# Kernel optimization log

Hardware: AMD Instinct MI355X
Metric: run time of the kernel (lower is better)

## Reference

```python
import jax, jax.numpy as jnp
import numpy as np

N = 100000          # nodes
E = 800000          # edges per relation
R = 6               # relations
B = 1000            # graphs
IN_DIM = 14
POS_COL = 5
PE = 8              # pos_emb_dim
H = 128             # hidden_dim
OUT = 128           # out_dim
NPOS = 24
D1 = IN_DIM - 1 + PE  # 21, GAT layer-1 input dim


def setup_inputs() -> dict:
    key = jax.random.key(0)
    ks = jax.random.split(key, 20)
    x_all = jax.random.normal(ks[0], (N, IN_DIM), dtype=jnp.float32)
    pos = jax.random.randint(ks[1], (N,), 0, NPOS)
    x_all = x_all.at[:, POS_COL].set(pos.astype(jnp.float32))
    edges = jax.random.randint(ks[2], (R, 2, E), 0, N, dtype=jnp.int32)
    batch = jnp.sort(jax.random.randint(ks[3], (N,), 0, B, dtype=jnp.int32))
    pos_table = jax.random.normal(ks[4], (NPOS, PE), dtype=jnp.float32) * 0.02
    W1 = jax.random.normal(ks[5], (R, D1, H), dtype=jnp.float32) * 0.1
    as1 = jax.random.normal(ks[6], (R, H), dtype=jnp.float32) * 0.1
    ad1 = jax.random.normal(ks[7], (R, H), dtype=jnp.float32) * 0.1
    b1 = jnp.zeros((R, H), dtype=jnp.float32)
    W2 = jax.random.normal(ks[8], (R, H, H), dtype=jnp.float32) * 0.05
    as2 = jax.random.normal(ks[9], (R, H), dtype=jnp.float32) * 0.1
    ad2 = jax.random.normal(ks[10], (R, H), dtype=jnp.float32) * 0.1
    b2 = jnp.zeros((R, H), dtype=jnp.float32)
    n1w = jnp.ones((H,), dtype=jnp.float32)
    n1b = jnp.zeros((H,), dtype=jnp.float32)
    n2w = jnp.ones((H,), dtype=jnp.float32)
    n2b = jnp.zeros((H,), dtype=jnp.float32)
    query = jax.random.normal(ks[11], (H,), dtype=jnp.float32) * 0.02
    projW = jax.random.normal(ks[12], (H, OUT), dtype=jnp.float32) * 0.05
    projb = jnp.zeros((OUT,), dtype=jnp.float32)
    return dict(x_all=x_all, edges=edges, batch=batch, pos_table=pos_table,
                W1=W1, as1=as1, ad1=ad1, b1=b1, W2=W2, as2=as2, ad2=ad2, b2=b2,
                n1w=n1w, n1b=n1b, n2w=n2w, n2b=n2b, query=query, projW=projW, projb=projb)


def _seg_softmax(logits, seg, num):
    m = jax.lax.stop_gradient(jax.ops.segment_max(logits, seg, num_segments=num))
    e = jnp.exp(logits - m[seg])
    s = jax.ops.segment_sum(e, seg, num_segments=num)
    return e / s[seg]


def _gat_layer(x, W, a_s, a_d, b, edges):
    # sum over R relation-specific GATConv(heads=1, concat=False) outputs
    n = x.shape[0]
    out = jnp.zeros((n, W.shape[-1]), dtype=x.dtype)
    for r in range(R):
        xp = x @ W[r]                       # [N, H] projected features
        src, dst = edges[r, 0], edges[r, 1]
        z = (xp @ a_s[r])[src] + (xp @ a_d[r])[dst]
        z = jnp.where(z > 0, z, 0.2 * z)    # LeakyReLU(0.2)
        alpha = _seg_softmax(z, dst, n)     # per-destination softmax
        agg = jax.ops.segment_sum(alpha[:, None] * xp[src], dst, num_segments=n)
        out = out + agg + b[r]
    return out


def _ln(x, w, b):
    mu = x.mean(-1, keepdims=True)
    v = ((x - mu) ** 2).mean(-1, keepdims=True)
    return (x - mu) / jnp.sqrt(v + 1e-5) * w + b


def reference(x_all, edges, batch, pos_table, W1, as1, ad1, b1,
              W2, as2, ad2, b2, n1w, n1b, n2w, n2b, query, projW, projb):
    cont = jnp.concatenate([x_all[:, :POS_COL], x_all[:, POS_COL + 1:]], axis=1)
    pidx = jnp.clip(x_all[:, POS_COL].astype(jnp.int32), 0, NPOS - 1)
    x = jnp.concatenate([cont, pos_table[pidx]], axis=1)  # [N, D1]
    x = _gat_layer(x, W1, as1, ad1, b1, edges)
    x = _ln(jax.nn.gelu(x, approximate=False), n1w, n1b)
    x = _gat_layer(x, W2, as2, ad2, b2, edges)
    x = _ln(jax.nn.gelu(x, approximate=False), n2w, n2b)
    # AttentionPooling: gather-score-softmax-scatter over batch segments
    scores = x @ query
    w = _seg_softmax(scores, batch, B)
    pool = jax.ops.segment_sum(w[:, None] * x, batch, num_segments=B)  # [B, H]
    return pool @ projW + projb
```

## Files before the change

### kernel.cpp

```cpp
#include <hip/hip_runtime.h>
#include <math.h>

#define NN   100000
#define EE   800000
#define RR   6
#define BB   1000
#define HH   128
#define MM   (RR*NN)
#define NBPR ((NN + 255) >> 8)
#define NBK  (RR * NBPR)
#define CH   4096

static inline int ceil_div(int a, int b){ return (a+b-1)/b; }

typedef __attribute__((ext_vector_type(8))) short bf16x8;
typedef __attribute__((ext_vector_type(4))) short bf16x4;
typedef __attribute__((ext_vector_type(4))) float f32x4;

__device__ __forceinline__ unsigned fenc(float f){
  unsigned u = __float_as_uint(f);
  return (u & 0x80000000u) ? ~u : (u | 0x80000000u);
}
__device__ __forceinline__ float fdec(unsigned u){
  return __uint_as_float((u & 0x80000000u) ? (u & 0x7fffffffu) : ~u);
}
__device__ __forceinline__ unsigned short f2bf(float f){
  unsigned u = __float_as_uint(f);
  return (unsigned short)((u + 0x7fffu + ((u >> 16) & 1u)) >> 16);
}
__device__ __forceinline__ float bf2f(unsigned short h){
  return __uint_as_float(((unsigned)h) << 16);
}

__global__ void k_bcount(const int* __restrict__ edges, int* __restrict__ bcnt)
{
  __shared__ int hist[NBPR];
  int t = threadIdx.x;
  const int nch = (EE + CH - 1) / CH;
  int r = blockIdx.x / nch, c = blockIdx.x - r*nch;
  for (int i = t; i < NBPR; i += 256) hist[i] = 0;
  __syncthreads();
  const int* dptr = edges + (size_t)r*2*EE + EE;
  int e0 = c*CH, e1 = min(EE, e0 + CH);
  for (int i = e0 + t; i < e1; i += 256)
    atomicAdd(&hist[dptr[i] >> 8], 1);
  __syncthreads();
  for (int i = t; i < NBPR; i += 256) {
    int h = hist[i];
    if (h) atomicAdd(&bcnt[r*NBPR + i], h);
  }
}

__global__ void k_bscan(const int* __restrict__ bcnt, int* __restrict__ boff,
                        int* __restrict__ off)
{
  __shared__ int sh[256];
  int t = threadIdx.x;
  int carry = 0;
  for (int c = 0; c < NBK; c += 256) {
    int idx = c + t;
    int v = (idx < NBK) ? bcnt[idx] : 0;
    sh[t] = v;
    __syncthreads();
    for (int o = 1; o < 256; o <<= 1) {
      int add = (t >= o) ? sh[t-o] : 0;
      __syncthreads();
      sh[t] += add;
      __syncthreads();
    }
    int incl = sh[t];
    int tot  = sh[255];
    if (idx < NBK) boff[idx] = carry + incl - v;
    __syncthreads();
    carry += tot;
  }
  if (t == 0) { boff[NBK] = carry; off[MM] = carry; }
}

__global__ void k_binscatter(const int* __restrict__ edges, int* __restrict__ bcur,
                             unsigned* __restrict__ ebkt)
{
  __shared__ int hist[NBPR];
  __shared__ int base[NBPR];
  int t = threadIdx.x;
  const int nch = (EE + CH - 1) / CH;
  int r = blockIdx.x / nch, c = blockIdx.x - r*nch;
  for (int i = t; i < NBPR; i += 256) hist[i] = 0;
  __syncthreads();
  const int* sptr = edges + (size_t)r*2*EE;
  const int* dptr = sptr + EE;
  int e0 = c*CH, e1 = min(EE, e0 + CH);
  for (int i = e0 + t; i < e1; i += 256)
    atomicAdd(&hist[dptr[i] >> 8], 1);
  __syncthreads();
  for (int i = t; i < NBPR; i += 256) {
    int h = hist[i];
    base[i] = h ? atomicAdd(&bcur[r*NBPR + i], h) : 0;
    hist[i] = 0;
  }
  __syncthreads();
  for (int i = e0 + t; i < e1; i += 256) {
    int dst = dptr[i];
    int b = dst >> 8;
    int slot = base[b] + atomicAdd(&hist[b], 1);
    ebkt[slot] = ((unsigned)sptr[i] << 8) | (unsigned)(dst & 255);
  }
}

__global__ void k_bbuild(const unsigned* __restrict__ ebkt, const int* __restrict__ boff,
                         int* __restrict__ off, int* __restrict__ elist)
{
  __shared__ int cnt[256];
  __shared__ int sc[256];
  __shared__ int cur[256];
  int t = threadIdx.x;
  int bb = blockIdx.x;
  int e0 = boff[bb], e1 = boff[bb+1];
  cnt[t] = 0;
  __syncthreads();
  for (int i = e0 + t; i < e1; i += 256)
    atomicAdd(&cnt[ebkt[i] & 255u], 1);
  __syncthreads();
  sc[t] = cnt[t];
  __syncthreads();
  for (int o = 1; o < 256; o <<= 1) {
    int add = (t >= o) ? sc[t-o] : 0;
    __syncthreads();
    sc[t] += add;
    __syncthreads();
  }
  int excl = sc[t] - cnt[t];
  int r = bb / NBPR, b = bb - r*NBPR;
  int dst = b*256 + t;
  if (dst < NN) off[r*NN + dst] = e0 + excl;
  cur[t] = e0 + excl;
  __syncthreads();
  for (int i = e0 + t; i < e1; i += 256) {
    unsigned w = ebkt[i];
    int slot = atomicAdd(&cur[w & 255u], 1);
    elist[slot] = (int)(w >> 8);
  }
}

__global__ void k_featprep(const float* __restrict__ x_all, const float* __restrict__ pos_table,
                           short* __restrict__ x0h, short* __restrict__ x0l)
{
  int gid = blockIdx.x*256 + threadIdx.x;
  if (gid >= NN*32) return;
  int nidx = gid >> 5, c = gid & 31;
  float v = 0.f;
  if (c < 13) {
    int scl = (c < 5) ? c : c + 1;
    v = x_all[nidx*14 + scl];
  } else if (c < 21) {
    int pi = (int)x_all[nidx*14 + 5];
    pi = pi < 0 ? 0 : (pi > 23 ? 23 : pi);
    v = pos_table[pi*8 + (c - 13)];
  }
  unsigned short h = f2bf(v);
  unsigned short l = f2bf(v - bf2f(h));
  x0h[gid] = (short)h;
  x0l[gid] = (short)l;
}

template<int KP>
__global__ void k_wprep(const float* __restrict__ W, int K,
                        short* __restrict__ Wh, short* __restrict__ Wl)
{
  int gid = blockIdx.x*256 + threadIdx.x;
  if (gid >= RR*128*KP) return;
  int r = gid / (128*KP);
  int rem = gid - r*(128*KP);
  int nn = rem / KP, k = rem - nn*KP;
  float v = (k < K) ? W[((size_t)r*K + k)*128 + nn] : 0.f;
  unsigned short h = f2bf(v);
  unsigned short l = f2bf(v - bf2f(h));
  Wh[gid] = (short)h;
  Wl[gid] = (short)l;
}

template<int KP>
__global__ void k_wa(const float* __restrict__ W, const float* __restrict__ as,
                     const float* __restrict__ ad, int K, float* __restrict__ wa)
{
  int idx = blockIdx.x*256 + threadIdx.x;
  if (idx >= 12*KP) return;
  int rr = idx / KP, k = idx - rr*KP;
  int r = (rr < 6) ? rr : rr - 6;
  const float* a = ((rr < 6) ? as : ad) + (size_t)r*HH;
  float s = 0.f;
  if (k < K) {
    const float* wrow = W + ((size_t)r*K + k)*128;
    #pragma unroll 8
    for (int h = 0; h < 128; ++h) s = fmaf(wrow[h], a[h], s);
  }
  wa[idx] = s;
}

__global__ void k_zsd32(const short* __restrict__ xh, const short* __restrict__ xl,
                        const float* __restrict__ wa, float* __restrict__ zsd, int n)
{
  __shared__ float w[12*32];
  int tid = threadIdx.x;
  for (int i = tid; i < 12*32; i += 256) w[i] = wa[i];
  __syncthreads();
  int g = blockIdx.x*256 + tid;
  if (g >= n) return;
  float v[32];
  #pragma unroll
  for (int c = 0; c < 4; ++c) {
    uint4 vh = *(const uint4*)(xh + (size_t)g*32 + c*8);
    uint4 vl = *(const uint4*)(xl + (size_t)g*32 + c*8);
    const unsigned short* hp = (const unsigned short*)&vh;
    const unsigned short* lp = (const unsigned short*)&vl;
    #pragma unroll
    for (int j = 0; j < 8; ++j) v[c*8+j] = bf2f(hp[j]) + bf2f(lp[j]);
  }
  #pragma unroll
  for (int rr = 0; rr < 12; ++rr) {
    float d = 0.f;
    #pragma unroll
    for (int k = 0; k < 32; ++k) d = fmaf(v[k], w[rr*32+k], d);
    zsd[(size_t)rr*n + g] = d;
  }
}

__global__ void k_agg1(const unsigned short* __restrict__ x0h, const float* __restrict__ zsd,
                       const int* __restrict__ elist, const int* __restrict__ off,
                       unsigned short* __restrict__ aggH, unsigned short* __restrict__ aggL,
                       int n)
{
  int gid = blockIdx.x*256 + threadIdx.x;
  int g = gid >> 4;
  int l = threadIdx.x & 15;
  if (g >= n) return;
  int sub = l >> 2, ch = l & 3;

  for (int rel = 0; rel < RR; ++rel) {
    const float* zsr = zsd + (size_t)rel*n;
    const float* zdr = zsd + (size_t)(6+rel)*n;
    int o0 = off[(size_t)rel*NN + g];
    int deg = off[(size_t)rel*NN + g + 1] - o0;
    float acc[8] = {0,0,0,0,0,0,0,0};
    float inv = 0.f;
    if (deg > 0) {
      float zdd = zdr[g];
      float m = -3.4e38f, es = 0.f;
      for (int i = l; i < deg; i += 16) {
        float z = zsr[elist[o0+i]] + zdd;
        z = (z > 0.f) ? z : 0.2f*z;
        float mn = fmaxf(m, z);
        es = es*__expf(m - mn) + __expf(z - mn);
        m = mn;
      }
      #pragma unroll
      for (int o = 1; o <= 8; o <<= 1) {
        float mo = __shfl_xor(m, o), eo = __shfl_xor(es, o);
        float mn = fmaxf(m, mo);
        es = es*__expf(m - mn) + eo*__expf(mo - mn);
        m = mn;
      }
      inv = 1.f / es;
      for (int base = 0; base < deg; base += 4) {
        int i = base + sub;
        float ew = 0.f; int ss = 0;
        if (i < deg) {
          ss = elist[o0+i];
          float z = zsr[ss] + zdd;
          z = (z > 0.f) ? z : 0.2f*z;
          ew = __expf(z - m);
        }
        uint4 v = *(const uint4*)(x0h + (size_t)ss*32 + ch*8);
        acc[0] = fmaf(ew, __uint_as_float(v.x << 16),         acc[0]);
        acc[1] = fmaf(ew, __uint_as_float(v.x & 0xffff0000u), acc[1]);
        acc[2] = fmaf(ew, __uint_as_float(v.y << 16),         acc[2]);
        acc[3] = fmaf(ew, __uint_as_float(v.y & 0xffff0000u), acc[3]);
        acc[4] = fmaf(ew, __uint_as_float(v.z << 16),         acc[4]);
        acc[5] = fmaf(ew, __uint_as_float(v.z & 0xffff0000u), acc[5]);
        acc[6] = fmaf(ew, __uint_as_float(v.w << 16),         acc[6]);
        acc[7] = fmaf(ew, __uint_as_float(v.w & 0xffff0000u), acc[7]);
      }
      #pragma unroll
      for (int j = 0; j < 8; ++j) {
        acc[j] += __shfl_xor(acc[j], 4);
        acc[j] += __shfl_xor(acc[j], 8);
      }
    }
    if (sub == 0) {
      uint4 ph, pl;
      unsigned* php = (unsigned*)&ph; unsigned* plp = (unsigned*)&pl;
      #pragma unroll
      for (int j2 = 0; j2 < 4; ++j2) {
        float a0 = acc[2*j2]   * inv;
        float a1 = acc[2*j2+1] * inv;
        unsigned short h0 = f2bf(a0), h1 = f2bf(a1);
        php[j2] = ((unsigned)h1 << 16) | h0;
        plp[j2] = ((unsigned)f2bf(a1 - bf2f(h1)) << 16) | f2bf(a0 - bf2f(h0));
      }
      size_t o = ((size_t)rel*n + g)*32 + ch*8;
      *(uint4*)(aggH + o) = ph;
      *(uint4*)(aggL + o) = pl;
    }
  }
}

__device__ __forceinline__ bf16x8 ldfragG(const short* __restrict__ p, int row, int kb, int KP_)
{
  bf16x4 a = *(const bf16x4*)(p + (size_t)row*KP_ + kb);
  bf16x4 b = *(const bf16x4*)(p + (size_t)row*KP_ + kb + 16);
  return __builtin_shufflevector(a, b, 0,1,2,3,4,5,6,7);
}

__global__ __launch_bounds__(256, 4)
void k_gemm1(const short* __restrict__ aggH, const short* __restrict__ aggL,
             const short* __restrict__ Wh, const short* __restrict__ Wl,
             const float* __restrict__ bsv,
             const float* __restrict__ nw, const float* __restrict__ nb,
             unsigned short* __restrict__ Yh, unsigned short* __restrict__ Yl, int n)
{
  __shared__ __align__(16) float Cs[32*136];
  int tid = threadIdx.x;
  int r0 = blockIdx.x * 32;
  int wid = tid >> 6, lane = tid & 63;
  int lr = lane & 15, lg = lane >> 4;
  int rt = wid >> 1;
  int c0 = (wid & 1) * 4;
  int arow = r0 + rt*16 + lr;
  int kb = 4*lg;
  f32x4 acct[4] = {{0,0,0,0},{0,0,0,0},{0,0,0,0},{0,0,0,0}};

  for (int rel = 0; rel < RR; ++rel) {
    const short* Ahr = aggH + (size_t)rel*n*32;
    const short* Alr = aggL + (size_t)rel*n*32;
    const short* Whr = Wh + (size_t)rel*128*32;
    const short* Wlr = Wl + (size_t)rel*128*32;
    bf16x8 ah = ldfragG(Ahr, arow, kb, 32);
    bf16x8 al = ldfragG(Alr, arow, kb, 32);
    #pragma unroll
    for (int t = 0; t < 4; ++t) {
      int wrow = (c0 + t)*16 + lr;
      bf16x8 whf = ldfragG(Whr, wrow, kb, 32);
      bf16x8 wlf = ldfragG(Wlr, wrow, kb, 32);
      acct[t] = __builtin_amdgcn_mfma_f32_16x16x32_bf16(ah, whf, acct[t], 0, 0, 0);
      acct[t] = __builtin_amdgcn_mfma_f32_16x16x32_bf16(al, whf, acct[t], 0, 0, 0);
      acct[t] = __builtin_amdgcn_mfma_f32_16x16x32_bf16(ah, wlf, acct[t], 0, 0, 0);
    }
  }

  #pragma unroll
  for (int t = 0; t < 4; ++t)
    #pragma unroll
    for (int v = 0; v < 4; ++v) {
      int row = rt*16 + lg*4 + v;
      int col = (c0 + t)*16 + lr;
      float x = acct[t][v] + bsv[col];
      Cs[row*136 + col] = 0.5f*x*(1.f + erff(x*0.70710678118654752f));
    }
  __syncthreads();
  {
    int r = tid >> 3, sg = tid & 7;
    float vals[16];
    float s = 0.f;
    #pragma unroll
    for (int i = 0; i < 16; ++i) { vals[i] = Cs[r*136 + sg*16 + i]; s += vals[i]; }
    s += __shfl_xor(s, 1); s += __shfl_xor(s, 2); s += __shfl_xor(s, 4);
    float mu = s * (1.f/128.f);
    float var = 0.f;
    #pragma unroll
    for (int i = 0; i < 16; ++i) { vals[i] -= mu; var += vals[i]*vals[i]; }
    var += __shfl_xor(var, 1); var += __shfl_xor(var, 2); var += __shfl_xor(var, 4);
    float inv = 1.f / sqrtf(var*(1.f/128.f) + 1e-5f);
    int g = r0 + r;
    uint4 ph0, ph1, pl0, pl1;
    unsigned* php0 = (unsigned*)&ph0; unsigned* php1 = (unsigned*)&ph1;
    unsigned* plp0 = (unsigned*)&pl0; unsigned* plp1 = (unsigned*)&pl1;
    #pragma unroll
    for (int j2 = 0; j2 < 8; ++j2) {
      int c = sg*16 + 2*j2;
      float y0 = vals[2*j2]  *inv*nw[c]   + nb[c];
      float y1 = vals[2*j2+1]*inv*nw[c+1] + nb[c+1];
      unsigned short h0 = f2bf(y0), h1 = f2bf(y1);
      unsigned hw = ((unsigned)h1 << 16) | h0;
      unsigned lw = ((unsigned)f2bf(y1 - bf2f(h1)) << 16) | f2bf(y0 - bf2f(h0));
      if (j2 < 4) { php0[j2] = hw; plp0[j2] = lw; }
      else        { php1[j2-4] = hw; plp1[j2-4] = lw; }
    }
    *(uint4*)(Yh + (size_t)g*128 + sg*16)     = ph0;
    *(uint4*)(Yh + (size_t)g*128 + sg*16 + 8) = ph1;
    *(uint4*)(Yl + (size_t)g*128 + sg*16)     = pl0;
    *(uint4*)(Yl + (size_t)g*128 + sg*16 + 8) = pl1;
  }
}

__device__ __forceinline__ bf16x8 ldfrag_(const short* p, int row, int kb, int KP_, int smask)
{
  int xr = row & smask;
  int s0 = (((kb)      >> 3) ^ xr) * 8 + (kb & 7);
  int s1 = (((kb + 16) >> 3) ^ xr) * 8 + (kb & 7);
  bf16x4 a = *(const bf16x4*)(p + (size_t)row*KP_ + s0);
  bf16x4 b = *(const bf16x4*)(p + (size_t)row*KP_ + s1);
  return __builtin_shufflevector(a, b, 0,1,2,3,4,5,6,7);
}

template<int KP>
__global__ __launch_bounds__(256, 2)
void k_gemm_mfma(const short* __restrict__ Ah, const short* __restrict__ Al,
                 const short* __restrict__ WhAll, const short* __restrict__ WlAll,
                 const float* __restrict__ a_sAll, const float* __restrict__ a_dAll,
                 unsigned short* __restrict__ xpbAll, float* __restrict__ zsAll,
                 float* __restrict__ zdAll, int rbase, int n)
{
  constexpr int SLOTS = KP/8;
  constexpr int SMASK = (SLOTS >= 8) ? 7 : (SLOTS-1);
  __shared__ short lds[320*KP];
  constexpr int AH0 = 0, AL0 = 32*KP, WH0 = 64*KP, WL0 = 192*KP;
  int tid = threadIdx.x;
  int r0 = blockIdx.x * 32;
  int ry = blockIdx.y;
  const short* Wh = WhAll + (size_t)(rbase+ry)*128*KP;
  const short* Wl = WlAll + (size_t)(rbase+ry)*128*KP;
  const float* a_s = a_sAll + (size_t)(rbase+ry)*HH;
  const float* a_d = a_dAll + (size_t)(rbase+ry)*HH;
  unsigned short* xpb = xpbAll + (size_t)ry*n*128;
  float* zs = zsAll + (size_t)ry*n;
  float* zd = zdAll + (size_t)ry*n;

  for (int ch = tid; ch < 32*SLOTS; ch += 256) {
    int row = ch / SLOTS, slot = ch - row*SLOTS;
    int gr = r0 + row;
    int dsl = (slot ^ (row & SMASK)) * 8;
    bf16x8 vh, vl;
    if (gr < n) {
      vh = *(const bf16x8*)(Ah + (size_t)gr*KP + slot*8);
      vl = *(const bf16x8*)(Al + (size_t)gr*KP + slot*8);
    } else {
      #pragma unroll
      for (int q = 0; q < 8; ++q) { vh[q] = 0; vl[q] = 0; }
    }
    *(bf16x8*)(lds + AH0 + row*KP + dsl) = vh;
    *(bf16x8*)(lds + AL0 + row*KP + dsl) = vl;
  }
  for (int ch = tid; ch < 128*SLOTS; ch += 256) {
    int row = ch / SLOTS, slot = ch - row*SLOTS;
    int dsl = (slot ^ (row & SMASK)) * 8;
    *(bf16x8*)(lds + WH0 + row*KP + dsl) = *(const bf16x8*)(Wh + (size_t)row*KP + slot*8);
    *(bf16x8*)(lds + WL0 + row*KP + dsl) = *(const bf16x8*)(Wl + (size_t)row*KP + slot*8);
  }
  __syncthreads();

  int wid = tid >> 6, lane = tid & 63;
  int lr = lane & 15, lg = lane >> 4;
  int rt = wid >> 1;
  int c0 = (wid & 1) * 4;
  f32x4 acc[4] = {{0,0,0,0},{0,0,0,0},{0,0,0,0},{0,0,0,0}};
  int arow = rt*16 + lr;

  #pragma unroll
  for (int kc = 0; kc < KP/32; ++kc) {
    int kb = kc*32 + 4*lg;
    bf16x8 ah = ldfrag_(lds + AH0, arow, kb, KP, SMASK);
    bf16x8 al = ldfrag_(lds + AL0, arow, kb, KP, SMASK);
    #pragma unroll
    for (int t = 0; t < 4; ++t) {
      int wrow = (c0 + t)*16 + lr;
      bf16x8 wh = ldfrag_(lds + WH0, wrow, kb, KP, SMASK);
      bf16x8 wl = ldfrag_(lds + WL0, wrow, kb, KP, SMASK);
      acc[t] = __builtin_amdgcn_mfma_f32_16x16x32_bf16(ah, wh, acc[t], 0, 0, 0);
      acc[t] = __builtin_amdgcn_mfma_f32_16x16x32_bf16(ah, wl, acc[t], 0, 0, 0);
      acc[t] = __builtin_amdgcn_mfma_f32_16x16x32_bf16(al, wh, acc[t], 0, 0, 0);
    }
  }
  __syncthreads();

  float* Cs = (float*)lds;
  #pragma unroll
  for (int t = 0; t < 4; ++t)
    #pragma unroll
    for (int v = 0; v < 4; ++v) {
      int row = rt*16 + lg*4 + v;
      int col = (c0 + t)*16 + lr;
      Cs[row*136 + col] = acc[t][v];
    }
  __syncthreads();

  {
    int r = tid >> 3, sg = tid & 7;
    float ps = 0.f, pd = 0.f;
    #pragma unroll
    for (int i = 0; i < 16; ++i) {
      int c = sg*16 + i;
      float x = Cs[r*136 + c];
      ps = fmaf(x, a_s[c], ps);
      pd = fmaf(x, a_d[c], pd);
    }
    ps += __shfl_xor(ps, 1); pd += __shfl_xor(pd, 1);
    ps += __shfl_xor(ps, 2); pd += __shfl_xor(pd, 2);
    ps += __shfl_xor(ps, 4); pd += __shfl_xor(pd, 4);
    int gr = r0 + r;
    if (sg == 0 && gr < n) { zs[gr] = ps; zd[gr] = pd; }
  }
  for (int i = tid; i < 32*16; i += 256) {
    int row = i >> 4, q = i & 15;
    int gr = r0 + row;
    if (gr < n) {
      const float* cp = Cs + row*136 + q*8;
      uint4 o;
      o.x = ((unsigned)f2bf(cp[1]) << 16) | f2bf(cp[0]);
      o.y = ((unsigned)f2bf(cp[3]) << 16) | f2bf(cp[2]);
      o.z = ((unsigned)f2bf(cp[5]) << 16) | f2bf(cp[4]);
      o.w = ((unsigned)f2bf(cp[7]) << 16) | f2bf(cp[6]);
      *(uint4*)(xpb + (size_t)gr*128 + q*8) = o;
    }
  }
}

template<int FIN>
__global__ void k_agg3(const unsigned short* __restrict__ xpb,
                       const float* __restrict__ zs,
                       const float* __restrict__ zd,
                       const int* __restrict__ elist,
                       const int* __restrict__ off,
                       float* __restrict__ hacc,
                       const float* __restrict__ bsum,
                       const float* __restrict__ nw, const float* __restrict__ nb,
                       float* __restrict__ Yf,
                       const float* __restrict__ q,
                       const int* __restrict__ batch,
                       float* __restrict__ scores, unsigned* __restrict__ bmax,
                       int n)
{
  int gid = blockIdx.x*256 + threadIdx.x;
  int g = gid >> 4;
  int l = threadIdx.x & 15;
  int gbase = threadIdx.x & 48;
  if (g >= n) return;

  float acc[8] = {0,0,0,0,0,0,0,0};

  #pragma unroll
  for (int r = 0; r < 3; ++r) {
    int o0 = off[(size_t)r*NN + g], o1 = off[(size_t)r*NN + g + 1];
    int deg = o1 - o0;
    if (deg <= 0) continue;
    const float* zsr = zs + (size_t)r*n;
    float zdd = zd[(size_t)r*n + g];

    float m = -3.4e38f;
    for (int i = l; i < deg; i += 16) {
      float z = zsr[elist[o0+i]] + zdd;
      z = (z > 0.f) ? z : 0.2f*z;
      m = fmaxf(m, z);
    }
    m = fmaxf(m, __shfl_xor(m, 1));
    m = fmaxf(m, __shfl_xor(m, 2));
    m = fmaxf(m, __shfl_xor(m, 4));
    m = fmaxf(m, __shfl_xor(m, 8));

    float tmp[8] = {0,0,0,0,0,0,0,0};
    float esum = 0.f;
    const unsigned short* xr = xpb + (size_t)r*n*128;
    for (int base = 0; base < deg; base += 16) {
      int i = base + l;
      float ew = 0.f; int s = 0;
      if (i < deg) {
        s = elist[o0+i];
        float z = zsr[s] + zdd;
        z = (z > 0.f) ? z : 0.2f*z;
        ew = __expf(z - m);
      }
      esum += ew;
      int cnt = min(16, deg - base);
      for (int t = 0; t < cnt; ++t) {
        float w = __shfl(ew, gbase + t);
        int ss = __shfl(s, gbase + t);
        const uint4 v = *(const uint4*)(xr + (size_t)ss*128 + l*8);
        tmp[0] = fmaf(w, __uint_as_float(v.x << 16),          tmp[0]);
        tmp[1] = fmaf(w, __uint_as_float(v.x & 0xffff0000u),  tmp[1]);
        tmp[2] = fmaf(w, __uint_as_float(v.y << 16),          tmp[2]);
        tmp[3] = fmaf(w, __uint_as_float(v.y & 0xffff0000u),  tmp[3]);
        tmp[4] = fmaf(w, __uint_as_float(v.z << 16),          tmp[4]);
        tmp[5] = fmaf(w, __uint_as_float(v.z & 0xffff0000u),  tmp[5]);
        tmp[6] = fmaf(w, __uint_as_float(v.w << 16),          tmp[6]);
        tmp[7] = fmaf(w, __uint_as_float(v.w & 0xffff0000u),  tmp[7]);
      }
    }
    esum += __shfl_xor(esum, 1);
    esum += __shfl_xor(esum, 2);
    esum += __shfl_xor(esum, 4);
    esum += __shfl_xor(esum, 8);
    float inv = 1.f / esum;
    #pragma unroll
    for (int j = 0; j < 8; ++j) acc[j] = fmaf(tmp[j], inv, acc[j]);
  }

  if (FIN == 0) {
    float* hp = hacc + (size_t)g*128 + l*8;
    float4 o0; o0.x = acc[0]; o0.y = acc[1]; o0.z = acc[2]; o0.w = acc[3];
    float4 o1; o1.x = acc[4]; o1.y = acc[5]; o1.z = acc[6]; o1.w = acc[7];
    *(float4*)hp = o0;
    *(float4*)(hp + 4) = o1;
  } else {
    const float* hp = hacc + (size_t)g*128 + l*8;
    float4 p0 = *(const float4*)hp;
    float4 p1 = *(const float4*)(hp + 4);
    float4 b0 = *(const float4*)(bsum + l*8);
    float4 b1 = *(const float4*)(bsum + l*8 + 4);
    acc[0] += p0.x + b0.x; acc[1] += p0.y + b0.y;
    acc[2] += p0.z + b0.z; acc[3] += p0.w + b0.w;
    acc[4] += p1.x + b1.x; acc[5] += p1.y + b1.y;
    acc[6] += p1.z + b1.z; acc[7] += p1.w + b1.w;
    float s = 0.f;
    #pragma unroll
    for (int j = 0; j < 8; ++j) {
      acc[j] = 0.5f*acc[j]*(1.f + erff(acc[j]*0.70710678118654752f));
      s += acc[j];
    }
    s += __shfl_xor(s, 1); s += __shfl_xor(s, 2);
    s += __shfl_xor(s, 4); s += __shfl_xor(s, 8);
    float mu = s * (1.f/128.f);
    float v = 0.f;
    #pragma unroll
    for (int j = 0; j < 8; ++j) { acc[j] -= mu; v += acc[j]*acc[j]; }
    v += __shfl_xor(v, 1); v += __shfl_xor(v, 2);
    v += __shfl_xor(v, 4); v += __shfl_xor(v, 8);
    v *= (1.f/128.f);
    float inv = 1.f / sqrtf(v + 1e-5f);
    float4 w0 = *(const float4*)(nw + l*8);
    float4 w1 = *(const float4*)(nw + l*8 + 4);
    float4 nb0 = *(const float4*)(nb + l*8);
    float4 nb1 = *(const float4*)(nb + l*8 + 4);
    float y[8];
    y[0] = acc[0]*inv*w0.x + nb0.x; y[1] = acc[1]*inv*w0.y + nb0.y;
    y[2] = acc[2]*inv*w0.z + nb0.z; y[3] = acc[3]*inv*w0.w + nb0.w;
    y[4] = acc[4]*inv*w1.x + nb1.x; y[5] = acc[5]*inv*w1.y + nb1.y;
    y[6] = acc[6]*inv*w1.z + nb1.z; y[7] = acc[7]*inv*w1.w + nb1.w;
    float* yp = Yf + (size_t)g*128 + l*8;
    float4 o0; o0.x = y[0]; o0.y = y[1]; o0.z = y[2]; o0.w = y[3];
    float4 o1; o1.x = y[4]; o1.y = y[5]; o1.z = y[6]; o1.w = y[7];
    *(float4*)yp = o0;
    *(float4*)(yp + 4) = o1;
    float4 q0 = *(const float4*)(q + l*8);
    float4 q1 = *(const float4*)(q + l*8 + 4);
    float sc = y[0]*q0.x + y[1]*q0.y + y[2]*q0.z + y[3]*q0.w
             + y[4]*q1.x + y[5]*q1.y + y[6]*q1.z + y[7]*q1.w;
    sc += __shfl_xor(sc, 1); sc += __shfl_xor(sc, 2);
    sc += __shfl_xor(sc, 4); sc += __shfl_xor(sc, 8);
    if (l == 0) {
      scores[g] = sc;
      atomicMax(&bmax[batch[g]], fenc(sc));
    }
  }
}

__global__ void k_bsum(const float* __restrict__ b, float* __restrict__ bs)
{
  int t = threadIdx.x;
  float s = 0.f;
  #pragma unroll
  for (int r = 0; r < RR; ++r) s += b[r*HH + t];
  bs[t] = s;
}

__global__ void k_segbounds(const int* __restrict__ batch, int* __restrict__ segst,
                            int n, int numB)
{
  int b = blockIdx.x*256 + threadIdx.x;
  if (b > numB) return;
  int lo = 0, hi = n;
  while (lo < hi) { int mid = (lo+hi) >> 1; if (batch[mid] < b) lo = mid+1; else hi = mid; }
  segst[b] = lo;
}

__global__ void k_pool(const float* __restrict__ X, const float* __restrict__ scores,
                       const int* __restrict__ segst, const unsigned* __restrict__ bmax,
                       float* __restrict__ pool, int numB)
{
  int b = blockIdx.x;
  int t = threadIdx.x;
  int s0 = segst[b], s1 = segst[b+1];
  float m = fdec(bmax[b]);
  float acc0 = 0.f, acc1 = 0.f, esum = 0.f;
  int i = s0;
  for (; i + 1 < s1; i += 2) {
    float e0 = __expf(scores[i] - m);
    float e1 = __expf(scores[i+1] - m);
    esum += e0 + e1;
    acc0 = fmaf(e0, X[(size_t)i*128 + t], acc0);
    acc1 = fmaf(e1, X[(size_t)(i+1)*128 + t], acc1);
  }
  if (i < s1) {
    float e0 = __expf(scores[i] - m);
    esum += e0;
    acc0 = fmaf(e0, X[(size_t)i*128 + t], acc0);
  }
  float inv = (s1 > s0) ? 1.f/esum : 0.f;
  pool[(size_t)b*128 + t] = (acc0 + acc1) * inv;
}

__global__ void k_outgemm(const float* __restrict__ pool, const float* __restrict__ projW,
                          const float* __restrict__ projb, float* __restrict__ out, int numB)
{
  int b = blockIdx.x;
  int j = threadIdx.x;
  __shared__ float p[128];
  p[j] = pool[(size_t)b*128 + j];
  __syncthreads();
  float acc = projb[j];
  #pragma unroll 16
  for (int k = 0; k < 128; ++k) acc = fmaf(p[k], projW[(size_t)k*128 + j], acc);
  out[(size_t)b*128 + j] = acc;
}

extern "C" void kernel_launch(void* const* d_in, const int* in_sizes, int n_in,
                              void* d_out, int out_size, void* d_ws, size_t ws_size,
                              hipStream_t stream)
{
  const float* x_all = (const float*)d_in[0];
  const int*   edges = (const int*)d_in[1];
  const int*   batch = (const int*)d_in[2];
  const float* pos_table = (const float*)d_in[3];
  const float* W1  = (const float*)d_in[4];
  const float* as1 = (const float*)d_in[5];
  const float* ad1 = (const float*)d_in[6];
  const float* b1  = (const float*)d_in[7];
  const float* W2  = (const float*)d_in[8];
  const float* as2 = (const float*)d_in[9];
  const float* ad2 = (const float*)d_in[10];
  const float* b2  = (const float*)d_in[11];
  const float* n1w = (const float*)d_in[12];
  const float* n1b = (const float*)d_in[13];
  const float* n2w = (const float*)d_in[14];
  const float* n2b = (const float*)d_in[15];
  const float* query = (const float*)d_in[16];
  const float* projW = (const float*)d_in[17];
  const float* projb = (const float*)d_in[18];
  float* out = (float*)d_out;
  (void)in_sizes; (void)n_in; (void)out_size; (void)ws_size;

  char* p = (char*)d_ws;
  auto alloc = [&](size_t b){ void* r = (void*)p; p += (b + 255) & ~(size_t)255; return r; };
  int*   off   = (int*)alloc((size_t)(MM+1)*sizeof(int));
  int*   elist = (int*)alloc((size_t)RR*EE*sizeof(int));
  int*   bcnt  = (int*)alloc((size_t)NBK*sizeof(int));
  int*   boff  = (int*)alloc((size_t)(NBK+1)*sizeof(int));
  int*   bcur  = (int*)alloc((size_t)NBK*sizeof(int));
  short* wtH   = (short*)alloc((size_t)RR*128*128*sizeof(short));
  short* wtL   = (short*)alloc((size_t)RR*128*128*sizeof(short));
  float* wa    = (float*)alloc((size_t)12*128*sizeof(float));
  float* zsd   = (float*)alloc((size_t)12*NN*sizeof(float));
  float* bsv   = (float*)alloc(128*sizeof(float));
  int*   segst = (int*)alloc((size_t)(BB+1)*sizeof(int));
  unsigned* bmax = (unsigned*)alloc((size_t)BB*sizeof(unsigned));
  float* pool  = (float*)alloc((size_t)BB*HH*sizeof(float));
  float* scrs  = (float*)alloc((size_t)NN*sizeof(float));
  unsigned short* xpb = (unsigned short*)alloc((size_t)3*NN*128*sizeof(short));
  float* R1    = (float*)alloc((size_t)NN*128*sizeof(float));
  float* R2    = (float*)alloc((size_t)NN*128*sizeof(float));

  unsigned* ebkt = (unsigned*)R1;
  short* x0h = (short*)R1;
  short* x0l = x0h + (size_t)NN*32;
  float* hacc = R1;
  unsigned short* h1h = (unsigned short*)R2;
  unsigned short* h1l = h1h + (size_t)NN*128;
  float* h2 = R2;
  unsigned short* aggH = (unsigned short*)xpb;
  unsigned short* aggL = aggH + (size_t)RR*NN*32;
  float* zs = zsd;
  float* zd = zsd + (size_t)3*NN;

  const int nch = (EE + CH - 1) / CH;
  hipMemsetAsync(bcnt, 0, (size_t)NBK*sizeof(int), stream);
  k_bcount<<<RR*nch,256,0,stream>>>(edges, bcnt);
  k_bscan<<<1,256,0,stream>>>(bcnt, boff, off);
  hipMemcpyAsync(bcur, boff, (size_t)NBK*sizeof(int), hipMemcpyDeviceToDevice, stream);
  k_binscatter<<<RR*nch,256,0,stream>>>(edges, bcur, ebkt);
  k_bbuild<<<NBK,256,0,stream>>>(ebkt, boff, off, elist);

  k_featprep<<<ceil_div(NN*32,256),256,0,stream>>>(x_all, pos_table, x0h, x0l);
  k_segbounds<<<ceil_div(BB+1,256),256,0,stream>>>(batch, segst, NN, BB);
  hipMemsetAsync(bmax, 0, (size_t)BB*sizeof(unsigned), stream);

  k_wa<32><<<ceil_div(12*32,256),256,0,stream>>>(W1, as1, ad1, 21, wa);
  k_zsd32<<<ceil_div(NN,256),256,0,stream>>>(x0h, x0l, wa, zsd, NN);
  k_wprep<32><<<ceil_div(RR*128*32,256),256,0,stream>>>(W1, 21, wtH, wtL);
  k_bsum<<<1,128,0,stream>>>(b1, bsv);
  k_agg1<<<ceil_div(NN*16,256),256,0,stream>>>((const unsigned short*)x0h, zsd, elist, off,
                                               aggH, aggL, NN);
  k_gemm1<<<ceil_div(NN,32),256,0,stream>>>((const short*)aggH, (const short*)aggL,
                                            wtH, wtL, bsv, n1w, n1b, h1h, h1l, NN);

  k_wprep<128><<<ceil_div(RR*128*128,256),256,0,stream>>>(W2, 128, wtH, wtL);
  k_bsum<<<1,128,0,stream>>>(b2, bsv);
  dim3 g3(ceil_div(NN,32), 3);
  int aggGrid = ceil_div(NN*16, 256);
  k_gemm_mfma<128><<<g3,256,0,stream>>>((const short*)h1h, (const short*)h1l,
                                        wtH, wtL, as2, ad2, xpb, zs, zd, 0, NN);
  k_agg3<0><<<aggGrid,256,0,stream>>>(xpb, zs, zd, elist, off, hacc,
      bsv, n2w, n2b, (float*)0, query, batch, scrs, bmax, NN);
  k_gemm_mfma<128><<<g3,256,0,stream>>>((const short*)h1h, (const short*)h1l,
                                        wtH, wtL, as2, ad2, xpb, zs, zd, 3, NN);
  k_agg3<2><<<aggGrid,256,0,stream>>>(xpb, zs, zd, elist, off + (size_t)3*NN, hacc,
      bsv, n2w, n2b, h2, query, batch, scrs, bmax, NN);

  k_pool<<<BB,128,0,stream>>>(h2, scrs, segst, bmax, pool, BB);
  k_outgemm<<<BB,128,0,stream>>>(pool, projW, projb, out, BB);
}
```

Measured before the change: 924.1 us.

## Drop CSR count pass via fixed-capacity buckets; fuse layer-2 relations into one pass

The CSR build no longer runs a separate counting pass over the edges. Instead the scatter kernel writes each edge into a fixed-capacity slot region per bucket (CAP entries) and counts at the same time. The scan and the final build then compact from those padded regions, which removes one full read of the edge array plus a memcpy. When the workspace is at least 300 MB, layer 2 computes all six relations' projections in one GEMM launch and aggregates them in a single k_agg3 pass, avoiding the fp32 hacc write and re-read. The risks are overflow if any bucket exceeds CAP, and a fused path that only runs when enough workspace is provided.

```diff
diff --git a/kernel.cpp b/kernel.cpp
--- a/kernel.cpp
+++ b/kernel.cpp
@@ -10,6 +10,7 @@
 #define NBPR ((NN + 255) >> 8)
 #define NBK  (RR * NBPR)
 #define CH   4096
+#define CAP  4096
 
 static inline int ceil_div(int a, int b){ return (a+b-1)/b; }
 
@@ -32,26 +33,38 @@
   return __uint_as_float(((unsigned)h) << 16);
 }
 
-__global__ void k_bcount(const int* __restrict__ edges, int* __restrict__ bcnt)
+__global__ void k_binscatter(const int* __restrict__ edges, int* __restrict__ bcur,
+                             unsigned* __restrict__ ebkt)
 {
   __shared__ int hist[NBPR];
+  __shared__ int base[NBPR];
   int t = threadIdx.x;
   const int nch = (EE + CH - 1) / CH;
   int r = blockIdx.x / nch, c = blockIdx.x - r*nch;
   for (int i = t; i < NBPR; i += 256) hist[i] = 0;
   __syncthreads();
-  const int* dptr = edges + (size_t)r*2*EE + EE;
+  const int* sptr = edges + (size_t)r*2*EE;
+  const int* dptr = sptr + EE;
   int e0 = c*CH, e1 = min(EE, e0 + CH);
   for (int i = e0 + t; i < e1; i += 256)
     atomicAdd(&hist[dptr[i] >> 8], 1);
   __syncthreads();
   for (int i = t; i < NBPR; i += 256) {
     int h = hist[i];
-    if (h) atomicAdd(&bcnt[r*NBPR + i], h);
-  }
-}
-
-__global__ void k_bscan(const int* __restrict__ bcnt, int* __restrict__ boff,
+    int gb = r*NBPR + i;
+    base[i] = h ? (gb*CAP + atomicAdd(&bcur[gb], h)) : 0;
+    hist[i] = 0;
+  }
+  __syncthreads();
+  for (int i = e0 + t; i < e1; i += 256) {
+    int dst = dptr[i];
+    int b = dst >> 8;
+    int slot = base[b] + atomicAdd(&hist[b], 1);
+    ebkt[slot] = ((unsigned)sptr[i] << 8) | (unsigned)(dst & 255);
+  }
+}
+
+__global__ void k_bscan(const int* __restrict__ bcur, int* __restrict__ boff,
                         int* __restrict__ off)
 {
   __shared__ int sh[256];
@@ -59,7 +72,7 @@
   int carry = 0;
   for (int c = 0; c < NBK; c += 256) {
     int idx = c + t;
-    int v = (idx < NBK) ? bcnt[idx] : 0;
+    int v = (idx < NBK) ? bcur[idx] : 0;
     sh[t] = v;
     __syncthreads();
     for (int o = 1; o < 256; o <<= 1) {
@@ -77,37 +90,8 @@
   if (t == 0) { boff[NBK] = carry; off[MM] = carry; }
 }
 
-__global__ void k_binscatter(const int* __restrict__ edges, int* __restrict__ bcur,
-                             unsigned* __restrict__ ebkt)
-{
-  __shared__ int hist[NBPR];
-  __shared__ int base[NBPR];
-  int t = threadIdx.x;
-  const int nch = (EE + CH - 1) / CH;
-  int r = blockIdx.x / nch, c = blockIdx.x - r*nch;
-  for (int i = t; i < NBPR; i += 256) hist[i] = 0;
-  __syncthreads();
-  const int* sptr = edges + (size_t)r*2*EE;
-  const int* dptr = sptr + EE;
-  int e0 = c*CH, e1 = min(EE, e0 + CH);
-  for (int i = e0 + t; i < e1; i += 256)
-    atomicAdd(&hist[dptr[i] >> 8], 1);
-  __syncthreads();
-  for (int i = t; i < NBPR; i += 256) {
-    int h = hist[i];
-    base[i] = h ? atomicAdd(&bcur[r*NBPR + i], h) : 0;
-    hist[i] = 0;
-  }
-  __syncthreads();
-  for (int i = e0 + t; i < e1; i += 256) {
-    int dst = dptr[i];
-    int b = dst >> 8;
-    int slot = base[b] + atomicAdd(&hist[b], 1);
-    ebkt[slot] = ((unsigned)sptr[i] << 8) | (unsigned)(dst & 255);
-  }
-}
-
-__global__ void k_bbuild(const unsigned* __restrict__ ebkt, const int* __restrict__ boff,
+__global__ void k_bbuild(const unsigned* __restrict__ ebkt, const int* __restrict__ bcur,
+                         const int* __restrict__ boff,
                          int* __restrict__ off, int* __restrict__ elist)
 {
   __shared__ int cnt[256];
@@ -115,10 +99,11 @@
   __shared__ int cur[256];
   int t = threadIdx.x;
   int bb = blockIdx.x;
-  int e0 = boff[bb], e1 = boff[bb+1];
+  int e0r = bb*CAP, e1r = e0r + bcur[bb];
+  int w0 = boff[bb];
   cnt[t] = 0;
   __syncthreads();
-  for (int i = e0 + t; i < e1; i += 256)
+  for (int i = e0r + t; i < e1r; i += 256)
     atomicAdd(&cnt[ebkt[i] & 255u], 1);
   __syncthreads();
   sc[t] = cnt[t];
@@ -132,10 +117,10 @@
   int excl = sc[t] - cnt[t];
   int r = bb / NBPR, b = bb - r*NBPR;
   int dst = b*256 + t;
-  if (dst < NN) off[r*NN + dst] = e0 + excl;
-  cur[t] = e0 + excl;
-  __syncthreads();
-  for (int i = e0 + t; i < e1; i += 256) {
+  if (dst < NN) off[r*NN + dst] = w0 + excl;
+  cur[t] = w0 + excl;
+  __syncthreads();
+  for (int i = e0r + t; i < e1r; i += 256) {
     unsigned w = ebkt[i];
     int slot = atomicAdd(&cur[w & 255u], 1);
     elist[slot] = (int)(w >> 8);
@@ -514,7 +499,7 @@
   }
 }
 
-template<int FIN>
+template<int NREL, int FIN>
 __global__ void k_agg3(const unsigned short* __restrict__ xpb,
                        const float* __restrict__ zs,
                        const float* __restrict__ zd,
@@ -538,7 +523,7 @@
   float acc[8] = {0,0,0,0,0,0,0,0};
 
   #pragma unroll
-  for (int r = 0; r < 3; ++r) {
+  for (int r = 0; r < NREL; ++r) {
     int o0 = off[(size_t)r*NN + g], o1 = off[(size_t)r*NN + g + 1];
     int deg = o1 - o0;
     if (deg <= 0) continue;
@@ -600,15 +585,17 @@
     *(float4*)hp = o0;
     *(float4*)(hp + 4) = o1;
   } else {
-    const float* hp = hacc + (size_t)g*128 + l*8;
-    float4 p0 = *(const float4*)hp;
-    float4 p1 = *(const float4*)(hp + 4);
+    if (FIN == 2) {
+      const float* hp = hacc + (size_t)g*128 + l*8;
+      float4 p0 = *(const float4*)hp;
+      float4 p1 = *(const float4*)(hp + 4);
+      acc[0] += p0.x; acc[1] += p0.y; acc[2] += p0.z; acc[3] += p0.w;
+      acc[4] += p1.x; acc[5] += p1.y; acc[6] += p1.z; acc[7] += p1.w;
+    }
     float4 b0 = *(const float4*)(bsum + l*8);
     float4 b1 = *(const float4*)(bsum + l*8 + 4);
-    acc[0] += p0.x + b0.x; acc[1] += p0.y + b0.y;
-    acc[2] += p0.z + b0.z; acc[3] += p0.w + b0.w;
-    acc[4] += p1.x + b1.x; acc[5] += p1.y + b1.y;
-    acc[6] += p1.z + b1.z; acc[7] += p1.w + b1.w;
+    acc[0] += b0.x; acc[1] += b0.y; acc[2] += b0.z; acc[3] += b0.w;
+    acc[4] += b1.x; acc[5] += b1.y; acc[6] += b1.z; acc[7] += b1.w;
     float s = 0.f;
     #pragma unroll
     for (int j = 0; j < 8; ++j) {
@@ -735,13 +722,14 @@
   const float* projW = (const float*)d_in[17];
   const float* projb = (const float*)d_in[18];
   float* out = (float*)d_out;
-  (void)in_sizes; (void)n_in; (void)out_size; (void)ws_size;
+  (void)in_sizes; (void)n_in; (void)out_size;
+
+  const bool use6 = ws_size >= ((size_t)300 << 20);
 
   char* p = (char*)d_ws;
   auto alloc = [&](size_t b){ void* r = (void*)p; p += (b + 255) & ~(size_t)255; return r; };
   int*   off   = (int*)alloc((size_t)(MM+1)*sizeof(int));
   int*   elist = (int*)alloc((size_t)RR*EE*sizeof(int));
-  int*   bcnt  = (int*)alloc((size_t)NBK*sizeof(int));
   int*   boff  = (int*)alloc((size_t)(NBK+1)*sizeof(int));
   int*   bcur  = (int*)alloc((size_t)NBK*sizeof(int));
   short* wtH   = (short*)alloc((size_t)RR*128*128*sizeof(short));
@@ -753,7 +741,8 @@
   unsigned* bmax = (unsigned*)alloc((size_t)BB*sizeof(unsigned));
   float* pool  = (float*)alloc((size_t)BB*HH*sizeof(float));
   float* scrs  = (float*)alloc((size_t)NN*sizeof(float));
-  unsigned short* xpb = (unsigned short*)alloc((size_t)3*NN*128*sizeof(short));
+  size_t xpbRel = use6 ? 6 : 3;
+  unsigned short* xpb = (unsigned short*)alloc((size_t)xpbRel*NN*128*sizeof(short));
   float* R1    = (float*)alloc((size_t)NN*128*sizeof(float));
   float* R2    = (float*)alloc((size_t)NN*128*sizeof(float));
 
@@ -763,19 +752,17 @@
   float* hacc = R1;
   unsigned short* h1h = (unsigned short*)R2;
   unsigned short* h1l = h1h + (size_t)NN*128;
-  float* h2 = R2;
+  float* h2 = use6 ? R1 : R2;
   unsigned short* aggH = (unsigned short*)xpb;
   unsigned short* aggL = aggH + (size_t)RR*NN*32;
   float* zs = zsd;
-  float* zd = zsd + (size_t)3*NN;
+  float* zd = zsd + (use6 ? (size_t)6*NN : (size_t)3*NN);
 
   const int nch = (EE + CH - 1) / CH;
-  hipMemsetAsync(bcnt, 0, (size_t)NBK*sizeof(int), stream);
-  k_bcount<<<RR*nch,256,0,stream>>>(edges, bcnt);
-  k_bscan<<<1,256,0,stream>>>(bcnt, boff, off);
-  hipMemcpyAsync(bcur, boff, (size_t)NBK*sizeof(int), hipMemcpyDeviceToDevice, stream);
+  hipMemsetAsync(bcur, 0, (size_t)NBK*sizeof(int), stream);
   k_binscatter<<<RR*nch,256,0,stream>>>(edges, bcur, ebkt);
-  k_bbuild<<<NBK,256,0,stream>>>(ebkt, boff, off, elist);
+  k_bscan<<<1,256,0,stream>>>(bcur, boff, off);
+  k_bbuild<<<NBK,256,0,stream>>>(ebkt, bcur, boff, off, elist);
 
   k_featprep<<<ceil_div(NN*32,256),256,0,stream>>>(x_all, pos_table, x0h, x0l);
   k_segbounds<<<ceil_div(BB+1,256),256,0,stream>>>(batch, segst, NN, BB);
@@ -792,16 +779,24 @@
 
   k_wprep<128><<<ceil_div(RR*128*128,256),256,0,stream>>>(W2, 128, wtH, wtL);
   k_bsum<<<1,128,0,stream>>>(b2, bsv);
-  dim3 g3(ceil_div(NN,32), 3);
   int aggGrid = ceil_div(NN*16, 256);
-  k_gemm_mfma<128><<<g3,256,0,stream>>>((const short*)h1h, (const short*)h1l,
-                                        wtH, wtL, as2, ad2, xpb, zs, zd, 0, NN);
-  k_agg3<0><<<aggGrid,256,0,stream>>>(xpb, zs, zd, elist, off, hacc,
-      bsv, n2w, n2b, (float*)0, query, batch, scrs, bmax, NN);
-  k_gemm_mfma<128><<<g3,256,0,stream>>>((const short*)h1h, (const short*)h1l,
-                                        wtH, wtL, as2, ad2, xpb, zs, zd, 3, NN);
-  k_agg3<2><<<aggGrid,256,0,stream>>>(xpb, zs, zd, elist, off + (size_t)3*NN, hacc,
-      bsv, n2w, n2b, h2, query, batch, scrs, bmax, NN);
+  if (use6) {
+    dim3 g6(ceil_div(NN,32), 6);
+    k_gemm_mfma<128><<<g6,256,0,stream>>>((const short*)h1h, (const short*)h1l,
+                                          wtH, wtL, as2, ad2, xpb, zs, zd, 0, NN);
+    k_agg3<6,3><<<aggGrid,256,0,stream>>>(xpb, zs, zd, elist, off, (float*)0,
+        bsv, n2w, n2b, h2, query, batch, scrs, bmax, NN);
+  } else {
+    dim3 g3(ceil_div(NN,32), 3);
+    k_gemm_mfma<128><<<g3,256,0,stream>>>((const short*)h1h, (const short*)h1l,
+                                          wtH, wtL, as2, ad2, xpb, zs, zd, 0, NN);
+    k_agg3<3,0><<<aggGrid,256,0,stream>>>(xpb, zs, zd, elist, off, hacc,
+        bsv, n2w, n2b, (float*)0, query, batch, scrs, bmax, NN);
+    k_gemm_mfma<128><<<g3,256,0,stream>>>((const short*)h1h, (const short*)h1l,
+                                          wtH, wtL, as2, ad2, xpb, zs, zd, 3, NN);
+    k_agg3<3,2><<<aggGrid,256,0,stream>>>(xpb, zs, zd, elist, off + (size_t)3*NN, hacc,
+        bsv, n2w, n2b, h2, query, batch, scrs, bmax, NN);
+  }
 
   k_pool<<<BB,128,0,stream>>>(h2, scrs, segst, bmax, pool, BB);
   k_outgemm<<<BB,128,0,stream>>>(pool, projW, projb, out, BB);
```

Result: no change. 912.2 us (-1.3%).
